# Optimization experiments

Hardware: AMD Instinct MI355X
Metric: run time of the kernel (lower is better)

## Reference

```python
import jax, jax.numpy as jnp
import numpy as np

B, D, TE, L, H = 4096, 1024, 256, 4, 8
HD = D // H
EPS = 1e-5


def _ln(x, g, b):
    m = x.mean(-1, keepdims=True)
    v = ((x - m) ** 2).mean(-1, keepdims=True)
    return (x - m) / jnp.sqrt(v + EPS) * g + b


def setup_inputs() -> dict:
    key = jax.random.key(0)
    ks = jax.random.split(key, 12)

    def n(k, shape, s=0.02):
        return jax.random.normal(k, shape, dtype=jnp.float32) * s

    return {
        "x": jax.random.normal(ks[0], (B, D), dtype=jnp.float32),
        "t_emb": jax.random.normal(ks[1], (B, TE), dtype=jnp.float32),
        "condition": jax.random.normal(ks[2], (B, D), dtype=jnp.float32),
        "in_w": n(ks[3], (D, D)), "in_b": jnp.zeros((D,), jnp.float32),
        "ln1_g": jnp.ones((L, D), jnp.float32), "ln1_b": jnp.zeros((L, D), jnp.float32),
        "wqkv": n(ks[4], (L, 3 * D, D)), "bqkv": jnp.zeros((L, 3 * D), jnp.float32),
        "wo": n(ks[5], (L, D, D)), "bo": jnp.zeros((L, D), jnp.float32),
        "ln2_g": jnp.ones((L, D), jnp.float32), "ln2_b": jnp.zeros((L, D), jnp.float32),
        "w1": n(ks[6], (L, 4 * D, D)), "b1": jnp.zeros((L, 4 * D), jnp.float32),
        "w2": n(ks[7], (L, D, 4 * D)), "b2": jnp.zeros((L, D), jnp.float32),
        "ada_w": n(ks[8], (L, 4 * D, TE)), "ada_b": jnp.zeros((L, 4 * D), jnp.float32),
        "out_ln_g": jnp.ones((D,), jnp.float32), "out_ln_b": jnp.zeros((D,), jnp.float32),
        "out_w": n(ks[9], (D, D)), "out_b": jnp.zeros((D,), jnp.float32),
    }


def reference(x, t_emb, condition, in_w, in_b, ln1_g, ln1_b, wqkv, bqkv, wo, bo,
              ln2_g, ln2_b, w1, b1, w2, b2, ada_w, ada_b,
              out_ln_g, out_ln_b, out_w, out_b):
    h = x @ in_w.T + in_b + condition              # [B, D]
    st = jax.nn.silu(t_emb)                        # adaLN input, shared across layers
    scale = 1.0 / jnp.sqrt(jnp.float32(HD))

    def block(h, p):
        l1g, l1b, wq, bq, woL, boL, l2g, l2b, w1L, b1L, w2L, b2L, awL, abL = p
        ada = st @ awL.T + abL                     # [B, 4D]
        s1, sh1, s2, sh2 = jnp.split(ada, 4, axis=-1)
        xn = _ln(h, l1g, l1b) * (1.0 + s1) + sh1
        qkv = xn @ wq.T + bq                       # [B, 3D]
        q, k, v = jnp.split(qkv, 3, axis=-1)
        qh = q.reshape(-1, H, HD)
        kh = k.reshape(-1, H, HD)
        vh = v.reshape(-1, H, HD)
        # seq_len == 1: one query, one key per head -> scalar score, softmax == 1
        score = jnp.einsum("bhd,bhd->bh", qh, kh) * scale
        attn = jnp.exp(score - score)              # exactly 1.0 (keeps grad path, matches torch)
        xa = (attn[..., None] * vh).reshape(-1, D) @ woL.T + boL
        h = h + xa
        xn = _ln(h, l2g, l2b) * (1.0 + s2) + sh2
        h = h + jax.nn.gelu(xn @ w1L.T + b1L, approximate=False) @ w2L.T + b2L
        return h, None

    params = (ln1_g, ln1_b, wqkv, bqkv, wo, bo, ln2_g, ln2_b, w1, b1, w2, b2, ada_w, ada_b)
    h, _ = jax.lax.scan(block, h, params)
    return _ln(h, out_ln_g, out_ln_b) @ out_w.T + out_b
```

## Files before the change

kernel.cpp:

```cpp
#include <hip/hip_runtime.h>
#include <hip/hip_bf16.h>

typedef __attribute__((ext_vector_type(8))) short short8;
typedef __attribute__((ext_vector_type(4))) float floatx4;
typedef unsigned short u16;

#define DEVI __device__ __forceinline__

DEVI u16 f2bf(float f) {
  union { float f; unsigned u; } v; v.f = f;
  unsigned r = v.u + 0x7fffu + ((v.u >> 16) & 1u);
  return (u16)(r >> 16);
}
DEVI float bf2f(u16 h) {
  union { unsigned u; float f; } v; v.u = (unsigned)h << 16; return v.f;
}

__global__ __launch_bounds__(256) void silu_kernel(const float* __restrict__ t,
                                                   u16* __restrict__ out) {
  const int i = blockIdx.x * 256 + threadIdx.x;
  float4 v = ((const float4*)t)[i];
  ushort4 o;
  o.x = f2bf(v.x / (1.f + expf(-v.x)));
  o.y = f2bf(v.y / (1.f + expf(-v.y)));
  o.z = f2bf(v.z / (1.f + expf(-v.z)));
  o.w = f2bf(v.w / (1.f + expf(-v.w)));
  ((ushort4*)out)[i] = o;
}

template<bool MOD>
__global__ __launch_bounds__(256)
void ln_kernel(const float* __restrict__ h, const float* __restrict__ g,
               const float* __restrict__ b, const u16* __restrict__ s1,
               const u16* __restrict__ sh1, u16* __restrict__ out) {
  const int row = blockIdx.x;
  const int tid = threadIdx.x;
  const float4 xv = ((const float4*)(h + (size_t)row * 1024))[tid];
  float sm = xv.x + xv.y + xv.z + xv.w;
  float sq = xv.x * xv.x + xv.y * xv.y + xv.z * xv.z + xv.w * xv.w;
  #pragma unroll
  for (int off = 32; off > 0; off >>= 1) {
    sm += __shfl_down(sm, off);
    sq += __shfl_down(sq, off);
  }
  __shared__ float red[10];
  if ((tid & 63) == 0) { red[tid >> 6] = sm; red[4 + (tid >> 6)] = sq; }
  __syncthreads();
  if (tid == 0) {
    float S = red[0] + red[1] + red[2] + red[3];
    float Q = red[4] + red[5] + red[6] + red[7];
    float mean = S * (1.f / 1024.f);
    float var  = Q * (1.f / 1024.f) - mean * mean;
    red[8] = mean;
    red[9] = 1.f / sqrtf(var + 1e-5f);
  }
  __syncthreads();
  const float mean = red[8], rstd = red[9];
  const float4 gv = ((const float4*)g)[tid];
  const float4 bv = ((const float4*)b)[tid];
  float y0 = (xv.x - mean) * rstd * gv.x + bv.x;
  float y1 = (xv.y - mean) * rstd * gv.y + bv.y;
  float y2 = (xv.z - mean) * rstd * gv.z + bv.z;
  float y3 = (xv.w - mean) * rstd * gv.w + bv.w;
  if (MOD) {
    const ushort4 sv  = ((const ushort4*)(s1  + (size_t)row * 4096))[tid];
    const ushort4 shv = ((const ushort4*)(sh1 + (size_t)row * 4096))[tid];
    y0 = y0 * (1.f + bf2f(sv.x)) + bf2f(shv.x);
    y1 = y1 * (1.f + bf2f(sv.y)) + bf2f(shv.y);
    y2 = y2 * (1.f + bf2f(sv.z)) + bf2f(shv.z);
    y3 = y3 * (1.f + bf2f(sv.w)) + bf2f(shv.w);
  }
  ushort4 o;
  o.x = f2bf(y0); o.y = f2bf(y1); o.z = f2bf(y2); o.w = f2bf(y3);
  ((ushort4*)(out + (size_t)row * 1024))[tid] = o;
}

template<int BM, int MODE, bool AF32>
__global__ __launch_bounds__(256, 2)
void gemm_kernel(const void* __restrict__ Av, const float* __restrict__ Bw,
                 const float* __restrict__ bias, const float* __restrict__ addsrc,
                 void* __restrict__ Cout, int M, int N, int K) {
  constexpr int BN = 128, BK = 64;
  constexpr int MI = BM / 32;
  constexpr int NI = 4;
  constexpr int NA = BM * 8 / 256;
  constexpr int NB = BN * 8 / 256;
  __shared__ u16 ldsA[BM * BK];
  __shared__ u16 ldsB[BN * BK];

  const int tid  = threadIdx.x;
  const int lane = tid & 63;
  const int wv   = tid >> 6;
  const int wr   = wv >> 1;
  const int wc   = wv & 1;
  const int r    = lane & 15;
  const int quad = lane >> 4;
  const int swz  = (r & 7) << 4;

  const int bm0 = blockIdx.y * BM;
  const int bn0 = blockIdx.x * BN;

  const int srow = tid >> 3;
  const int scol = tid & 7;

  floatx4 acc[MI][NI] = {};

  float4 af0[NA], af1[NA];
  short8 ab[NA];
  float4 bf0[NB], bf1[NB];

  auto load_tile = [&](int k0) {
    #pragma unroll
    for (int i = 0; i < NA; ++i) {
      const int row = srow + 32 * i;
      if constexpr (AF32) {
        const float* gp = (const float*)Av + (size_t)(bm0 + row) * K + k0 + scol * 8;
        af0[i] = *(const float4*)gp;
        af1[i] = *(const float4*)(gp + 4);
      } else {
        const u16* gp = (const u16*)Av + (size_t)(bm0 + row) * K + k0 + scol * 8;
        ab[i] = *(const short8*)gp;
      }
    }
    #pragma unroll
    for (int i = 0; i < NB; ++i) {
      const int row = srow + 32 * i;
      const float* gp = Bw + (size_t)(bn0 + row) * K + k0 + scol * 8;
      bf0[i] = *(const float4*)gp;
      bf1[i] = *(const float4*)(gp + 4);
    }
  };

  auto write_lds = [&]() {
    #pragma unroll
    for (int i = 0; i < NA; ++i) {
      const int row = srow + 32 * i;
      short8 w;
      if constexpr (AF32) {
        w[0] = (short)f2bf(af0[i].x); w[1] = (short)f2bf(af0[i].y);
        w[2] = (short)f2bf(af0[i].z); w[3] = (short)f2bf(af0[i].w);
        w[4] = (short)f2bf(af1[i].x); w[5] = (short)f2bf(af1[i].y);
        w[6] = (short)f2bf(af1[i].z); w[7] = (short)f2bf(af1[i].w);
      } else {
        w = ab[i];
      }
      *(short8*)((char*)ldsA + row * 128 + ((scol ^ (row & 7)) << 4)) = w;
    }
    #pragma unroll
    for (int i = 0; i < NB; ++i) {
      const int row = srow + 32 * i;
      short8 w;
      w[0] = (short)f2bf(bf0[i].x); w[1] = (short)f2bf(bf0[i].y);
      w[2] = (short)f2bf(bf0[i].z); w[3] = (short)f2bf(bf0[i].w);
      w[4] = (short)f2bf(bf1[i].x); w[5] = (short)f2bf(bf1[i].y);
      w[6] = (short)f2bf(bf1[i].z); w[7] = (short)f2bf(bf1[i].w);
      *(short8*)((char*)ldsB + row * 128 + ((scol ^ (row & 7)) << 4)) = w;
    }
  };

  const int nt = K / BK;
  load_tile(0);
  for (int t = 0; t < nt; ++t) {
    write_lds();
    __syncthreads();
    if (t + 1 < nt) load_tile((t + 1) * BK);
    #pragma unroll
    for (int ks = 0; ks < 2; ++ks) {
      const int off = ((ks << 6) + (quad << 4)) ^ swz;
      short8 afr[MI], bfr[NI];
      #pragma unroll
      for (int m = 0; m < MI; ++m) {
        const int row = wr * (BM / 2) + m * 16 + r;
        afr[m] = *(const short8*)((const char*)ldsA + row * 128 + off);
      }
      #pragma unroll
      for (int n = 0; n < NI; ++n) {
        const int row = wc * 64 + n * 16 + r;
        bfr[n] = *(const short8*)((const char*)ldsB + row * 128 + off);
      }
      #pragma unroll
      for (int m = 0; m < MI; ++m)
        #pragma unroll
        for (int n = 0; n < NI; ++n)
          acc[m][n] = __builtin_amdgcn_mfma_f32_16x16x32_bf16(afr[m], bfr[n],
                                                              acc[m][n], 0, 0, 0);
    }
    __syncthreads();
  }

  const int colb  = bn0 + wc * 64;
  const int rowb0 = bm0 + wr * (BM / 2);
  #pragma unroll
  for (int n = 0; n < NI; ++n) {
    const int cn = colb + n * 16 + r;
    const float bv = bias[cn];
    #pragma unroll
    for (int m = 0; m < MI; ++m) {
      const int rowb = rowb0 + m * 16 + quad * 4;
      #pragma unroll
      for (int j = 0; j < 4; ++j) {
        const size_t idx = (size_t)(rowb + j) * N + cn;
        float val = acc[m][n][j] + bv;
        if constexpr (MODE == 0) {
          ((u16*)Cout)[idx] = f2bf(val);
        } else if constexpr (MODE == 1) {
          if (addsrc) val += addsrc[idx];
          ((float*)Cout)[idx] = val;
        } else {
          val = 0.5f * val * (1.f + erff(val * 0.70710678118654752f));
          ((u16*)Cout)[idx] = f2bf(val);
        }
      }
    }
  }
}

extern "C" void kernel_launch(void* const* d_in, const int* in_sizes, int n_in,
                              void* d_out, int out_size, void* d_ws, size_t ws_size,
                              hipStream_t stream) {
  (void)in_sizes; (void)n_in; (void)out_size; (void)ws_size;
  const float* x     = (const float*)d_in[0];
  const float* t_emb = (const float*)d_in[1];
  const float* cond  = (const float*)d_in[2];
  const float* in_w  = (const float*)d_in[3];
  const float* in_b  = (const float*)d_in[4];
  const float* ln1_g = (const float*)d_in[5];
  const float* ln1_b = (const float*)d_in[6];
  const float* wqkv  = (const float*)d_in[7];
  const float* bqkv  = (const float*)d_in[8];
  const float* wo    = (const float*)d_in[9];
  const float* bo    = (const float*)d_in[10];
  const float* ln2_g = (const float*)d_in[11];
  const float* ln2_b = (const float*)d_in[12];
  const float* w1    = (const float*)d_in[13];
  const float* b1    = (const float*)d_in[14];
  const float* w2    = (const float*)d_in[15];
  const float* b2    = (const float*)d_in[16];
  const float* ada_w = (const float*)d_in[17];
  const float* ada_b = (const float*)d_in[18];
  const float* oln_g = (const float*)d_in[19];
  const float* oln_b = (const float*)d_in[20];
  const float* out_w = (const float*)d_in[21];
  const float* out_b = (const float*)d_in[22];
  float* out = (float*)d_out;

  char* p = (char*)d_ws;
  auto alloc = [&](size_t n) { char* r = p; p += (n + 255) & ~(size_t)255; return r; };
  u16*   stb = (u16*)  alloc((size_t)4096 * 256  * 2);
  float* h   = (float*)alloc((size_t)4096 * 1024 * 4);
  u16*   ada = (u16*)  alloc((size_t)4096 * 4096 * 2);
  u16*   a1  = ada;
  u16*   xn  = (u16*)  alloc((size_t)4096 * 1024 * 2);
  u16*   vb  = (u16*)  alloc((size_t)4096 * 1024 * 2);

  silu_kernel<<<1024, 256, 0, stream>>>(t_emb, stb);

  gemm_kernel<64, 1, true><<<dim3(8, 64), 256, 0, stream>>>(
      x, in_w, in_b, cond, h, 4096, 1024, 1024);

  for (int l = 0; l < 4; ++l) {
    gemm_kernel<128, 0, false><<<dim3(32, 32), 256, 0, stream>>>(
        stb, ada_w + (size_t)l * 1048576, ada_b + l * 4096, nullptr, ada,
        4096, 4096, 256);
    ln_kernel<true><<<4096, 256, 0, stream>>>(h, ln1_g + l * 1024, ln1_b + l * 1024,
                                              ada, ada + 1024, xn);
    gemm_kernel<64, 0, false><<<dim3(8, 64), 256, 0, stream>>>(
        xn, wqkv + (size_t)l * 3145728 + 2097152, bqkv + l * 3072 + 2048,
        nullptr, vb, 4096, 1024, 1024);
    gemm_kernel<64, 1, false><<<dim3(8, 64), 256, 0, stream>>>(
        vb, wo + (size_t)l * 1048576, bo + l * 1024, h, h, 4096, 1024, 1024);
    ln_kernel<true><<<4096, 256, 0, stream>>>(h, ln2_g + l * 1024, ln2_b + l * 1024,
                                              ada + 2048, ada + 3072, xn);
    gemm_kernel<128, 2, false><<<dim3(32, 32), 256, 0, stream>>>(
        xn, w1 + (size_t)l * 4194304, b1 + l * 4096, nullptr, a1,
        4096, 4096, 1024);
    gemm_kernel<64, 1, false><<<dim3(8, 64), 256, 0, stream>>>(
        a1, w2 + (size_t)l * 4194304, b2 + l * 1024, h, h, 4096, 1024, 4096);
  }
  ln_kernel<false><<<4096, 256, 0, stream>>>(h, oln_g, oln_b, nullptr, nullptr, xn);
  gemm_kernel<64, 1, false><<<dim3(8, 64), 256, 0, stream>>>(
      xn, out_w, out_b, nullptr, out, 4096, 1024, 1024);
}
```

Before: 1.391 ms.

## Add split-K with atomic accumulation for residual GEMMs

Adds a K-split grid dimension to the GEMM kernel and a new epilogue mode that atomically accumulates partial results into the fp32 residual buffer. Block z==0 adds bias and the optional add source. The in-projection, attention output and FFN down-projection GEMMs are split 2 or 4 ways to fill more compute units, and the residual buffer is zeroed up front. This trades better occupancy for atomic read-modify-write traffic and nondeterministic summation order.

```diff
diff --git a/kernel.cpp b/kernel.cpp
--- a/kernel.cpp
+++ b/kernel.cpp
@@ -79,7 +79,7 @@
 __global__ __launch_bounds__(256, 2)
 void gemm_kernel(const void* __restrict__ Av, const float* __restrict__ Bw,
                  const float* __restrict__ bias, const float* __restrict__ addsrc,
-                 void* __restrict__ Cout, int M, int N, int K) {
+                 void* __restrict__ Cout, int M, int N, int K, int Kc) {
   constexpr int BN = 128, BK = 64;
   constexpr int MI = BM / 32;
   constexpr int NI = 4;
@@ -97,8 +97,9 @@
   const int quad = lane >> 4;
   const int swz  = (r & 7) << 4;
 
-  const int bm0 = blockIdx.y * BM;
-  const int bn0 = blockIdx.x * BN;
+  const int bm0  = blockIdx.y * BM;
+  const int bn0  = blockIdx.x * BN;
+  const int koff = blockIdx.z * Kc;
 
   const int srow = tid >> 3;
   const int scol = tid & 7;
@@ -158,12 +159,12 @@
     }
   };
 
-  const int nt = K / BK;
-  load_tile(0);
+  const int nt = Kc / BK;
+  load_tile(koff);
   for (int t = 0; t < nt; ++t) {
     write_lds();
     __syncthreads();
-    if (t + 1 < nt) load_tile((t + 1) * BK);
+    if (t + 1 < nt) load_tile(koff + (t + 1) * BK);
     #pragma unroll
     for (int ks = 0; ks < 2; ++ks) {
       const int off = ((ks << 6) + (quad << 4)) ^ swz;
@@ -200,15 +201,23 @@
       #pragma unroll
       for (int j = 0; j < 4; ++j) {
         const size_t idx = (size_t)(rowb + j) * N + cn;
-        float val = acc[m][n][j] + bv;
+        float val = acc[m][n][j];
         if constexpr (MODE == 0) {
-          ((u16*)Cout)[idx] = f2bf(val);
+          ((u16*)Cout)[idx] = f2bf(val + bv);
         } else if constexpr (MODE == 1) {
+          val += bv;
           if (addsrc) val += addsrc[idx];
           ((float*)Cout)[idx] = val;
-        } else {
+        } else if constexpr (MODE == 2) {
+          val += bv;
           val = 0.5f * val * (1.f + erff(val * 0.70710678118654752f));
           ((u16*)Cout)[idx] = f2bf(val);
+        } else {
+          if (blockIdx.z == 0) {
+            val += bv;
+            if (addsrc) val += addsrc[idx];
+          }
+          atomicAdd((float*)Cout + idx, val);
         }
       }
     }
@@ -253,31 +262,35 @@
   u16*   xn  = (u16*)  alloc((size_t)4096 * 1024 * 2);
   u16*   vb  = (u16*)  alloc((size_t)4096 * 1024 * 2);
 
+  hipMemsetAsync(h, 0, (size_t)4096 * 1024 * 4, stream);
+
   silu_kernel<<<1024, 256, 0, stream>>>(t_emb, stb);
 
-  gemm_kernel<64, 1, true><<<dim3(8, 64), 256, 0, stream>>>(
-      x, in_w, in_b, cond, h, 4096, 1024, 1024);
+  gemm_kernel<64, 3, true><<<dim3(8, 64, 2), 256, 0, stream>>>(
+      x, in_w, in_b, cond, h, 4096, 1024, 1024, 512);
 
   for (int l = 0; l < 4; ++l) {
-    gemm_kernel<128, 0, false><<<dim3(32, 32), 256, 0, stream>>>(
+    gemm_kernel<128, 0, false><<<dim3(32, 32, 1), 256, 0, stream>>>(
         stb, ada_w + (size_t)l * 1048576, ada_b + l * 4096, nullptr, ada,
-        4096, 4096, 256);
+        4096, 4096, 256, 256);
     ln_kernel<true><<<4096, 256, 0, stream>>>(h, ln1_g + l * 1024, ln1_b + l * 1024,
                                               ada, ada + 1024, xn);
-    gemm_kernel<64, 0, false><<<dim3(8, 64), 256, 0, stream>>>(
+    gemm_kernel<64, 0, false><<<dim3(8, 64, 1), 256, 0, stream>>>(
         xn, wqkv + (size_t)l * 3145728 + 2097152, bqkv + l * 3072 + 2048,
-        nullptr, vb, 4096, 1024, 1024);
-    gemm_kernel<64, 1, false><<<dim3(8, 64), 256, 0, stream>>>(
-        vb, wo + (size_t)l * 1048576, bo + l * 1024, h, h, 4096, 1024, 1024);
+        nullptr, vb, 4096, 1024, 1024, 1024);
+    gemm_kernel<64, 3, false><<<dim3(8, 64, 2), 256, 0, stream>>>(
+        vb, wo + (size_t)l * 1048576, bo + l * 1024, nullptr, h,
+        4096, 1024, 1024, 512);
     ln_kernel<true><<<4096, 256, 0, stream>>>(h, ln2_g + l * 1024, ln2_b + l * 1024,
                                               ada + 2048, ada + 3072, xn);
-    gemm_kernel<128, 2, false><<<dim3(32, 32), 256, 0, stream>>>(
+    gemm_kernel<128, 2, false><<<dim3(32, 32, 1), 256, 0, stream>>>(
         xn, w1 + (size_t)l * 4194304, b1 + l * 4096, nullptr, a1,
-        4096, 4096, 1024);
-    gemm_kernel<64, 1, false><<<dim3(8, 64), 256, 0, stream>>>(
-        a1, w2 + (size_t)l * 4194304, b2 + l * 1024, h, h, 4096, 1024, 4096);
+        4096, 4096, 1024, 1024);
+    gemm_kernel<64, 3, false><<<dim3(8, 64, 4), 256, 0, stream>>>(
+        a1, w2 + (size_t)l * 4194304, b2 + l * 1024, nullptr, h,
+        4096, 1024, 4096, 1024);
   }
   ln_kernel<false><<<4096, 256, 0, stream>>>(h, oln_g, oln_b, nullptr, nullptr, xn);
-  gemm_kernel<64, 1, false><<<dim3(8, 64), 256, 0, stream>>>(
-      xn, out_w, out_b, nullptr, out, 4096, 1024, 1024);
-}
+  gemm_kernel<64, 1, false><<<dim3(8, 64, 1), 256, 0, stream>>>(
+      xn, out_w, out_b, nullptr, out, 4096, 1024, 1024, 1024);
+}
```

Result: no change. 1.415 ms (+1.7%).
